# Kernel optimization log

Measured on AMD Instinct MI355X. Metric: run time of the kernel, lower is better.

## Reference

```python
import jax, jax.numpy as jnp
import numpy as np

N = 100000          # number of active sparse points
GRID = 800          # coordinate grid extent (2D)
KS = 9              # 3x3 kernel offsets
C_IN = 24
C_HID = 144         # round(24 * 6)
C_OUT = 24
EPS = 1e-5


def _build_kernel_map():
    """Build MinkowskiEngine-style kernel map for a 3x3 stride-1 channelwise conv.
    Returns (in_idx, out_idx, off_id), each [KS*N] int32. Invalid (no neighbor)
    entries point to sentinel row N so the padded gather/scatter is a no-op."""
    rng = np.random.default_rng(0)
    flat = rng.choice(GRID * GRID, size=N, replace=False)  # unique 2D coords
    ys, xs = flat // GRID, flat % GRID
    coord_to_idx = -np.ones(GRID * GRID, dtype=np.int64)
    coord_to_idx[flat] = np.arange(N)
    in_chunks, out_chunks, off_chunks = [], [], []
    pts = np.arange(N, dtype=np.int64)
    k = 0
    for dy in (-1, 0, 1):
        for dx in (-1, 0, 1):
            ny, nx = ys + dy, xs + dx
            inside = (ny >= 0) & (ny < GRID) & (nx >= 0) & (nx < GRID)
            nflat = np.clip(ny, 0, GRID - 1) * GRID + np.clip(nx, 0, GRID - 1)
            nidx = np.where(inside, coord_to_idx[nflat], -1)
            valid = nidx >= 0
            in_chunks.append(np.where(valid, nidx, N))
            out_chunks.append(np.where(valid, pts, N))
            off_chunks.append(np.full(N, k, dtype=np.int64))
            k += 1
    in_idx = np.concatenate(in_chunks).astype(np.int32)
    out_idx = np.concatenate(out_chunks).astype(np.int32)
    off_id = np.concatenate(off_chunks).astype(np.int32)
    return in_idx, out_idx, off_id


def setup_inputs() -> dict:
    key = jax.random.key(0)
    ks = jax.random.split(key, 4)
    in_idx, out_idx, off_id = _build_kernel_map()
    return {
        "feats": jax.random.normal(ks[0], (N, C_IN), jnp.float32),
        "w1": jax.random.normal(ks[1], (C_IN, C_HID), jnp.float32) * 0.1,
        "g1": jnp.ones((C_HID,), jnp.float32),
        "b1": jnp.zeros((C_HID,), jnp.float32),
        "w2": jax.random.normal(ks[2], (KS, C_HID), jnp.float32) * 0.1,
        "g2": jnp.ones((C_HID,), jnp.float32),
        "b2": jnp.zeros((C_HID,), jnp.float32),
        "w3": jax.random.normal(ks[3], (C_HID, C_OUT), jnp.float32) * 0.1,
        "g3": jnp.ones((C_OUT,), jnp.float32),
        "b3": jnp.zeros((C_OUT,), jnp.float32),
        "in_idx": jnp.asarray(in_idx),
        "out_idx": jnp.asarray(out_idx),
        "off_id": jnp.asarray(off_id),
    }


def _bn(x, g, b):
    # MinkowskiBatchNorm forward (training mode): per-channel stats over points
    m = jnp.mean(x, axis=0)
    v = jnp.var(x, axis=0)
    return (x - m) * jax.lax.rsqrt(v + EPS) * g + b


def _relu6(x):
    return jnp.clip(x, 0.0, 6.0)


def _channelwise_conv3x3(x, w2, in_idx, out_idx, off_id):
    # gather-multiply-scatter: out[p, c] = sum_k w2[k, c] * x[nbr_k(p), c]
    xp = jnp.concatenate([x, jnp.zeros((1, x.shape[1]), x.dtype)], axis=0)  # sentinel row
    contrib = xp[in_idx] * w2[off_id]                     # [KS*N, C_HID]
    out = jnp.zeros((N + 1, x.shape[1]), x.dtype).at[out_idx].add(contrib)
    return out[:N]


def reference(feats, w1, g1, b1, w2, g2, b2, w3, g3, b3, in_idx, out_idx, off_id):
    x = _relu6(_bn(feats @ w1, g1, b1))                   # 1x1 expand
    x = _relu6(_bn(_channelwise_conv3x3(x, w2, in_idx, out_idx, off_id), g2, b2))
    x = _bn(x @ w3, g3, b3)                               # 1x1 project
    return x + feats                                      # residual (in==out, stride==1)
```

## Files before the change

### kernel.cpp

```cpp
#include <hip/hip_runtime.h>

#define N_PTS 100000
#define KSZ 9
#define C_IN 24
#define C_HID 144
#define C_OUT 24
#define G4_HID 36
#define G4_OUT 6
#define EPSV 1e-5f

#define X1N_OFF   0
#define X1N_SIZE  ((N_PTS + 1) * C_HID)
#define X2_OFF    (X1N_OFF + X1N_SIZE)
#define X2_SIZE   (N_PTS * C_HID)
#define ST_OFF    (X2_OFF + X2_SIZE)
#define MU1_O     (ST_OFF + 0)
#define M1_O      (ST_OFF + 32)
#define SC1_O     (ST_OFF + 640)
#define SH1_O     (ST_OFF + 800)
#define SUM2_O    (ST_OFF + 960)
#define SQ2_O     (ST_OFF + 1120)
#define SC2_O     (ST_OFF + 1280)
#define SH2_O     (ST_OFF + 1440)
#define SUM3_O    (ST_OFF + 1600)
#define SQ3_O     (ST_OFF + 1632)
#define SC3_O     (ST_OFF + 1664)
#define SH3_O     (ST_OFF + 1696)
#define ST_SIZE   1728
#define Y3_OFF    0

__device__ inline float4 f4z() { return make_float4(0.f, 0.f, 0.f, 0.f); }
__device__ inline float4 f4_add(float4 a, float4 b) {
    return make_float4(a.x + b.x, a.y + b.y, a.z + b.z, a.w + b.w);
}
__device__ inline float4 f4_fma4(float4 a, float4 b, float4 c) {
    return make_float4(fmaf(a.x, b.x, c.x), fmaf(a.y, b.y, c.y),
                       fmaf(a.z, b.z, c.z), fmaf(a.w, b.w, c.w));
}
__device__ inline float4 f4_fma_s(float s, float4 b, float4 c) {
    return make_float4(fmaf(s, b.x, c.x), fmaf(s, b.y, c.y),
                       fmaf(s, b.z, c.z), fmaf(s, b.w, c.w));
}
__device__ inline float4 f4_clamp6(float4 a) {
    return make_float4(fminf(fmaxf(a.x, 0.f), 6.f), fminf(fmaxf(a.y, 0.f), 6.f),
                       fminf(fmaxf(a.z, 0.f), 6.f), fminf(fmaxf(a.w, 0.f), 6.f));
}
__device__ inline float f4_get(const float4& v, int e) {
    return e == 0 ? v.x : (e == 1 ? v.y : (e == 2 ? v.z : v.w));
}

__global__ void k_init(float* ws) {
    int t = threadIdx.x;
    for (int i = t; i < ST_SIZE; i += 256) ws[ST_OFF + i] = 0.f;
    if (t < C_HID) ws[X1N_OFF + (size_t)N_PTS * C_HID + t] = 0.f;
}

#define MROWS 128
__device__ inline float task_acc(const float* tile, int cnt, int task) {
    if (task < 576) {
        int i = task / 24, j = task % 24;
        float a = 0.f;
        for (int r = 0; r < cnt; r++) a += tile[r * 24 + i] * tile[r * 24 + j];
        return a;
    }
    int k = task - 576;
    float a = 0.f;
    for (int r = 0; r < cnt; r++) a += tile[r * 24 + k];
    return a;
}
__global__ void k_moments(const float* __restrict__ feats, float* __restrict__ ws) {
    __shared__ float tile[MROWS * C_IN];
    int t = threadIdx.x;
    float acc0 = 0.f, acc1 = 0.f, acc2 = 0.f;
    int nChunks = (N_PTS + MROWS - 1) / MROWS;
    for (int ch = blockIdx.x; ch < nChunks; ch += gridDim.x) {
        int r0 = ch * MROWS;
        int cnt = min(MROWS, N_PTS - r0);
        __syncthreads();
        for (int e = t; e < cnt * C_IN; e += 256) tile[e] = feats[(size_t)r0 * C_IN + e];
        __syncthreads();
        acc0 += task_acc(tile, cnt, t);
        acc1 += task_acc(tile, cnt, t + 256);
        if (t < 88) acc2 += task_acc(tile, cnt, t + 512);
    }
    {
        int task = t;
        atomicAdd(&ws[M1_O + task], acc0);
    }
    {
        int task = t + 256;
        atomicAdd(&ws[M1_O + task], acc1);
    }
    if (t < 88) {
        int task = t + 512;
        if (task < 576) atomicAdd(&ws[M1_O + task], acc2);
        else            atomicAdd(&ws[MU1_O + task - 576], acc2);
    }
}

__global__ void k_fin1(const float* __restrict__ w1, const float* __restrict__ g1,
                       const float* __restrict__ b1, float* __restrict__ ws) {
    int c = threadIdx.x;
    if (c >= C_HID) return;
    float wc[C_IN];
    for (int k = 0; k < C_IN; k++) wc[k] = w1[k * C_HID + c];
    const float invN = 1.f / (float)N_PTS;
    float mean = 0.f;
    for (int k = 0; k < C_IN; k++) mean += ws[MU1_O + k] * wc[k];
    mean *= invN;
    float e2 = 0.f;
    for (int i = 0; i < C_IN; i++) {
        float s = 0.f;
        for (int j = 0; j < C_IN; j++) s += ws[M1_O + i * 24 + j] * wc[j];
        e2 += wc[i] * s;
    }
    e2 *= invN;
    float var = e2 - mean * mean;
    float s1 = g1[c] * rsqrtf(var + EPSV);
    ws[SC1_O + c] = s1;
    ws[SH1_O + c] = b1[c] - mean * s1;
}

__global__ void k_gemm1(const float* __restrict__ feats, const float* __restrict__ w1,
                        float* __restrict__ ws) {
    __shared__ float4 w1s[C_IN * G4_HID];
    __shared__ float4 sc[G4_HID], sh[G4_HID];
    int t = threadIdx.x;
    const float4* w1v = (const float4*)w1;
    for (int e = t; e < C_IN * G4_HID; e += 256) w1s[e] = w1v[e];
    if (t < G4_HID) {
        sc[t] = ((const float4*)(ws + SC1_O))[t];
        sh[t] = ((const float4*)(ws + SH1_O))[t];
    }
    __syncthreads();
    float4* x1v = (float4*)(ws + X1N_OFF);
    const int T = N_PTS * G4_HID;
    for (int tau = blockIdx.x * 256 + t; tau < T; tau += gridDim.x * 256) {
        int p = tau / G4_HID;
        int g = tau % G4_HID;
        const float4* fr = (const float4*)(feats + (size_t)p * C_IN);
        float4 acc = f4z();
#pragma unroll
        for (int q = 0; q < 6; q++) {
            float4 fq = fr[q];
            acc = f4_fma_s(fq.x, w1s[(4 * q + 0) * G4_HID + g], acc);
            acc = f4_fma_s(fq.y, w1s[(4 * q + 1) * G4_HID + g], acc);
            acc = f4_fma_s(fq.z, w1s[(4 * q + 2) * G4_HID + g], acc);
            acc = f4_fma_s(fq.w, w1s[(4 * q + 3) * G4_HID + g], acc);
        }
        x1v[tau] = f4_clamp6(f4_fma4(acc, sc[g], sh[g]));
    }
}

__global__ void k_conv(const float* __restrict__ w2, const int* __restrict__ in_idx,
                       float* __restrict__ ws) {
    __shared__ float4 w2s[KSZ * G4_HID];
    __shared__ float lsum[C_HID], lsq[C_HID];
    int t = threadIdx.x;
    for (int e = t; e < KSZ * G4_HID; e += 256) w2s[e] = ((const float4*)w2)[e];
    if (t < C_HID) { lsum[t] = 0.f; lsq[t] = 0.f; }
    __syncthreads();
    const float4* x1v = (const float4*)(ws + X1N_OFF);
    float4* x2v = (float4*)(ws + X2_OFF);
    bool active = t < 252;
    int pt = t / 36, g = t % 36;
    float4 rs = f4z(), rq = f4z();
    int nChunks = (N_PTS + 6) / 7;
    for (int ch = blockIdx.x; ch < nChunks; ch += gridDim.x) {
        int p = ch * 7 + pt;
        if (active && p < N_PTS) {
            int idxs[KSZ];
#pragma unroll
            for (int k = 0; k < KSZ; k++) idxs[k] = in_idx[k * N_PTS + p];
            float4 acc = f4z();
#pragma unroll
            for (int k = 0; k < KSZ; k++) {
                float4 v = x1v[(size_t)idxs[k] * G4_HID + g];
                acc = f4_fma4(w2s[k * G4_HID + g], v, acc);
            }
            x2v[(size_t)p * G4_HID + g] = acc;
            rs = f4_add(rs, acc);
            rq = f4_fma4(acc, acc, rq);
        }
    }
    if (active) {
        atomicAdd(&lsum[4 * g + 0], rs.x); atomicAdd(&lsum[4 * g + 1], rs.y);
        atomicAdd(&lsum[4 * g + 2], rs.z); atomicAdd(&lsum[4 * g + 3], rs.w);
        atomicAdd(&lsq[4 * g + 0], rq.x);  atomicAdd(&lsq[4 * g + 1], rq.y);
        atomicAdd(&lsq[4 * g + 2], rq.z);  atomicAdd(&lsq[4 * g + 3], rq.w);
    }
    __syncthreads();
    if (t < C_HID) {
        atomicAdd(&ws[SUM2_O + t], lsum[t]);
        atomicAdd(&ws[SQ2_O + t], lsq[t]);
    }
}

__global__ void k_fin2(const float* __restrict__ g2, const float* __restrict__ b2,
                       float* __restrict__ ws) {
    int c = threadIdx.x;
    if (c >= C_HID) return;
    const float invN = 1.f / (float)N_PTS;
    float mean = ws[SUM2_O + c] * invN;
    float var = ws[SQ2_O + c] * invN - mean * mean;
    float s = g2[c] * rsqrtf(var + EPSV);
    ws[SC2_O + c] = s;
    ws[SH2_O + c] = b2[c] - mean * s;
}

__global__ void k_gemm2(const float* __restrict__ w3, float* __restrict__ ws) {
    __shared__ float4 w3s[C_HID * G4_OUT];
    __shared__ float4 sc2[G4_HID], sh2[G4_HID];
    int t = threadIdx.x;
    for (int e = t; e < C_HID * G4_OUT; e += 256) w3s[e] = ((const float4*)w3)[e];
    if (t < G4_HID) {
        sc2[t] = ((const float4*)(ws + SC2_O))[t];
        sh2[t] = ((const float4*)(ws + SH2_O))[t];
    }
    __syncthreads();
    const float4* x2v = (const float4*)(ws + X2_OFF);
    float4* y3v = (float4*)(ws + Y3_OFF);
    int gtid = blockIdx.x * 256 + t;
    int r0 = gtid * 2, r1 = r0 + 1;
    bool v0 = r0 < N_PTS, v1 = r1 < N_PTS;
    float4 a0[G4_OUT], a1[G4_OUT];
#pragma unroll
    for (int c4 = 0; c4 < G4_OUT; c4++) { a0[c4] = f4z(); a1[c4] = f4z(); }
    for (int h4 = 0; h4 < G4_HID; h4++) {
        float4 xa = v0 ? x2v[(size_t)r0 * G4_HID + h4] : f4z();
        float4 xb = v1 ? x2v[(size_t)r1 * G4_HID + h4] : f4z();
        float4 s = sc2[h4], b = sh2[h4];
        xa = f4_clamp6(f4_fma4(xa, s, b));
        xb = f4_clamp6(f4_fma4(xb, s, b));
#pragma unroll
        for (int e = 0; e < 4; e++) {
            int h = h4 * 4 + e;
            float fa = f4_get(xa, e), fb = f4_get(xb, e);
#pragma unroll
            for (int c4 = 0; c4 < G4_OUT; c4++) {
                float4 w = w3s[h * G4_OUT + c4];
                a0[c4] = f4_fma_s(fa, w, a0[c4]);
                a1[c4] = f4_fma_s(fb, w, a1[c4]);
            }
        }
    }
    if (v0) {
#pragma unroll
        for (int c4 = 0; c4 < G4_OUT; c4++) y3v[(size_t)r0 * G4_OUT + c4] = a0[c4];
    }
    if (v1) {
#pragma unroll
        for (int c4 = 0; c4 < G4_OUT; c4++) y3v[(size_t)r1 * G4_OUT + c4] = a1[c4];
    }
}

__global__ void k_red3(float* __restrict__ ws) {
    int t = threadIdx.x;
    const float* y3 = ws + Y3_OFF;
    float rs = 0.f, rq = 0.f;
    const int total = N_PTS * C_OUT;
    for (int e = blockIdx.x * 192 + t; e < total; e += gridDim.x * 192) {
        float v = y3[e];
        rs += v; rq += v * v;
    }
    __shared__ float ls[192], lq[192];
    ls[t] = rs; lq[t] = rq;
    __syncthreads();
    if (t < C_OUT) {
        float s = 0.f, q = 0.f;
        for (int u = t; u < 192; u += C_OUT) { s += ls[u]; q += lq[u]; }
        atomicAdd(&ws[SUM3_O + t], s);
        atomicAdd(&ws[SQ3_O + t], q);
    }
}

__global__ void k_fin3(const float* __restrict__ g3, const float* __restrict__ b3,
                       float* __restrict__ ws) {
    int c = threadIdx.x;
    if (c >= C_OUT) return;
    const float invN = 1.f / (float)N_PTS;
    float mean = ws[SUM3_O + c] * invN;
    float var = ws[SQ3_O + c] * invN - mean * mean;
    float s = g3[c] * rsqrtf(var + EPSV);
    ws[SC3_O + c] = s;
    ws[SH3_O + c] = b3[c] - mean * s;
}

__global__ void k_out(const float* __restrict__ feats, const float* __restrict__ ws,
                      float* __restrict__ out) {
    int t4 = blockIdx.x * 256 + threadIdx.x;
    const int T = N_PTS * G4_OUT;
    if (t4 >= T) return;
    int g = t4 % G4_OUT;
    float4 y = ((const float4*)(ws + Y3_OFF))[t4];
    float4 s = ((const float4*)(ws + SC3_O))[g];
    float4 b = ((const float4*)(ws + SH3_O))[g];
    float4 f = ((const float4*)feats)[t4];
    ((float4*)out)[t4] = f4_add(f4_fma4(y, s, b), f);
}

extern "C" void kernel_launch(void* const* d_in, const int* in_sizes, int n_in,
                              void* d_out, int out_size, void* d_ws, size_t ws_size,
                              hipStream_t stream) {
    const float* feats = (const float*)d_in[0];
    const float* w1 = (const float*)d_in[1];
    const float* g1 = (const float*)d_in[2];
    const float* b1 = (const float*)d_in[3];
    const float* w2 = (const float*)d_in[4];
    const float* g2 = (const float*)d_in[5];
    const float* b2 = (const float*)d_in[6];
    const float* w3 = (const float*)d_in[7];
    const float* g3 = (const float*)d_in[8];
    const float* b3 = (const float*)d_in[9];
    const int* in_idx = (const int*)d_in[10];
    float* ws = (float*)d_ws;
    float* out = (float*)d_out;

    hipLaunchKernelGGL(k_init, dim3(1), dim3(256), 0, stream, ws);
    hipLaunchKernelGGL(k_moments, dim3(256), dim3(256), 0, stream, feats, ws);
    hipLaunchKernelGGL(k_fin1, dim3(1), dim3(192), 0, stream, w1, g1, b1, ws);
    hipLaunchKernelGGL(k_gemm1, dim3(2048), dim3(256), 0, stream, feats, w1, ws);
    hipLaunchKernelGGL(k_conv, dim3(2048), dim3(256), 0, stream, w2, in_idx, ws);
    hipLaunchKernelGGL(k_fin2, dim3(1), dim3(192), 0, stream, g2, b2, ws);
    hipLaunchKernelGGL(k_gemm2, dim3((N_PTS + 511) / 512), dim3(256), 0, stream, w3, ws);
    hipLaunchKernelGGL(k_red3, dim3(512), dim3(192), 0, stream, ws);
    hipLaunchKernelGGL(k_fin3, dim3(1), dim3(64), 0, stream, g3, b3, ws);
    hipLaunchKernelGGL(k_out, dim3((N_PTS * G4_OUT + 255) / 256), dim3(256), 0, stream,
                       feats, ws, out);
}
```

Measured before the change: 281.3 us.

## Store intermediates in fp16, fold BN finalize kernels, prefetch conv indices

The expanded and convolved hidden activations are now stored as fp16 instead of fp32, halving the bytes moved by the gather-heavy conv and by gemm2. The three single-block BN finalize kernels are folded into their consumer kernels, and gemm1 keeps BN-scaled weights in registers with one channel per thread. k_moments reads feats straight from global memory with contiguous row ranges per block, and k_conv software-prefetches the next chunk's neighbor indices and uses nontemporal stores. The cost is lower precision on intermediates and per-block recomputation of the BN scale and shift.

```diff
diff --git a/kernel.cpp b/kernel.cpp
--- a/kernel.cpp
+++ b/kernel.cpp
@@ -1,267 +1,259 @@
 #include <hip/hip_runtime.h>
+#include <hip/hip_fp16.h>
 
 #define N_PTS 100000
 #define KSZ 9
 #define C_IN 24
 #define C_HID 144
 #define C_OUT 24
-#define G4_HID 36
-#define G4_OUT 6
 #define EPSV 1e-5f
 
-#define X1N_OFF   0
-#define X1N_SIZE  ((N_PTS + 1) * C_HID)
-#define X2_OFF    (X1N_OFF + X1N_SIZE)
-#define X2_SIZE   (N_PTS * C_HID)
-#define ST_OFF    (X2_OFF + X2_SIZE)
-#define MU1_O     (ST_OFF + 0)
-#define M1_O      (ST_OFF + 32)
-#define SC1_O     (ST_OFF + 640)
-#define SH1_O     (ST_OFF + 800)
-#define SUM2_O    (ST_OFF + 960)
-#define SQ2_O     (ST_OFF + 1120)
-#define SC2_O     (ST_OFF + 1280)
-#define SH2_O     (ST_OFF + 1440)
-#define SUM3_O    (ST_OFF + 1600)
-#define SQ3_O     (ST_OFF + 1632)
-#define SC3_O     (ST_OFF + 1664)
-#define SH3_O     (ST_OFF + 1696)
-#define ST_SIZE   1728
-#define Y3_OFF    0
+#define X1N_B 0ull
+#define X2_B  28800512ull
+#define ST_B  57600512ull
+#define Y3_B  0ull
+
+#define MU1_F  0
+#define M1_F   32
+#define SUM2_F 640
+#define SQ2_F  800
+#define SUM3_F 960
+#define SQ3_F  992
+#define ST_FLOATS 1024
+
+typedef float f4v __attribute__((ext_vector_type(4)));
 
 __device__ inline float4 f4z() { return make_float4(0.f, 0.f, 0.f, 0.f); }
-__device__ inline float4 f4_add(float4 a, float4 b) {
-    return make_float4(a.x + b.x, a.y + b.y, a.z + b.z, a.w + b.w);
-}
-__device__ inline float4 f4_fma4(float4 a, float4 b, float4 c) {
-    return make_float4(fmaf(a.x, b.x, c.x), fmaf(a.y, b.y, c.y),
-                       fmaf(a.z, b.z, c.z), fmaf(a.w, b.w, c.w));
-}
 __device__ inline float4 f4_fma_s(float s, float4 b, float4 c) {
     return make_float4(fmaf(s, b.x, c.x), fmaf(s, b.y, c.y),
                        fmaf(s, b.z, c.z), fmaf(s, b.w, c.w));
 }
-__device__ inline float4 f4_clamp6(float4 a) {
-    return make_float4(fminf(fmaxf(a.x, 0.f), 6.f), fminf(fmaxf(a.y, 0.f), 6.f),
-                       fminf(fmaxf(a.z, 0.f), 6.f), fminf(fmaxf(a.w, 0.f), 6.f));
-}
-__device__ inline float f4_get(const float4& v, int e) {
-    return e == 0 ? v.x : (e == 1 ? v.y : (e == 2 ? v.z : v.w));
-}
-
-__global__ void k_init(float* ws) {
-    int t = threadIdx.x;
-    for (int i = t; i < ST_SIZE; i += 256) ws[ST_OFF + i] = 0.f;
-    if (t < C_HID) ws[X1N_OFF + (size_t)N_PTS * C_HID + t] = 0.f;
-}
-
-#define MROWS 128
-__device__ inline float task_acc(const float* tile, int cnt, int task) {
-    if (task < 576) {
-        int i = task / 24, j = task % 24;
-        float a = 0.f;
-        for (int r = 0; r < cnt; r++) a += tile[r * 24 + i] * tile[r * 24 + j];
-        return a;
-    }
-    int k = task - 576;
+__device__ inline float clamp6(float x) { return fminf(fmaxf(x, 0.f), 6.f); }
+
+__global__ void k_init(char* wsb) {
+    int t = threadIdx.x;
+    float* STF = (float*)(wsb + ST_B);
+    for (int i = t; i < ST_FLOATS; i += 256) STF[i] = 0.f;
+    float* sent = (float*)(wsb + X1N_B + (size_t)N_PTS * (C_HID * 2));
+    if (t < 72) sent[t] = 0.f;
+}
+
+__global__ void k_moments(const float* __restrict__ feats, char* __restrict__ wsb) {
+    int t = threadIdx.x;
+    float* STF = (float*)(wsb + ST_B);
+    int len = (N_PTS + gridDim.x - 1) / gridDim.x;
+    int r0 = blockIdx.x * len;
+    int r1 = min(r0 + len, N_PTS);
+    if (t >= 600) return;
     float a = 0.f;
-    for (int r = 0; r < cnt; r++) a += tile[r * 24 + k];
-    return a;
-}
-__global__ void k_moments(const float* __restrict__ feats, float* __restrict__ ws) {
-    __shared__ float tile[MROWS * C_IN];
-    int t = threadIdx.x;
-    float acc0 = 0.f, acc1 = 0.f, acc2 = 0.f;
-    int nChunks = (N_PTS + MROWS - 1) / MROWS;
-    for (int ch = blockIdx.x; ch < nChunks; ch += gridDim.x) {
-        int r0 = ch * MROWS;
-        int cnt = min(MROWS, N_PTS - r0);
-        __syncthreads();
-        for (int e = t; e < cnt * C_IN; e += 256) tile[e] = feats[(size_t)r0 * C_IN + e];
-        __syncthreads();
-        acc0 += task_acc(tile, cnt, t);
-        acc1 += task_acc(tile, cnt, t + 256);
-        if (t < 88) acc2 += task_acc(tile, cnt, t + 512);
-    }
-    {
-        int task = t;
-        atomicAdd(&ws[M1_O + task], acc0);
-    }
-    {
-        int task = t + 256;
-        atomicAdd(&ws[M1_O + task], acc1);
-    }
-    if (t < 88) {
-        int task = t + 512;
-        if (task < 576) atomicAdd(&ws[M1_O + task], acc2);
-        else            atomicAdd(&ws[MU1_O + task - 576], acc2);
-    }
-}
-
-__global__ void k_fin1(const float* __restrict__ w1, const float* __restrict__ g1,
-                       const float* __restrict__ b1, float* __restrict__ ws) {
-    int c = threadIdx.x;
-    if (c >= C_HID) return;
-    float wc[C_IN];
-    for (int k = 0; k < C_IN; k++) wc[k] = w1[k * C_HID + c];
-    const float invN = 1.f / (float)N_PTS;
-    float mean = 0.f;
-    for (int k = 0; k < C_IN; k++) mean += ws[MU1_O + k] * wc[k];
-    mean *= invN;
-    float e2 = 0.f;
-    for (int i = 0; i < C_IN; i++) {
-        float s = 0.f;
-        for (int j = 0; j < C_IN; j++) s += ws[M1_O + i * 24 + j] * wc[j];
-        e2 += wc[i] * s;
-    }
-    e2 *= invN;
-    float var = e2 - mean * mean;
-    float s1 = g1[c] * rsqrtf(var + EPSV);
-    ws[SC1_O + c] = s1;
-    ws[SH1_O + c] = b1[c] - mean * s1;
-}
-
-__global__ void k_gemm1(const float* __restrict__ feats, const float* __restrict__ w1,
-                        float* __restrict__ ws) {
-    __shared__ float4 w1s[C_IN * G4_HID];
-    __shared__ float4 sc[G4_HID], sh[G4_HID];
-    int t = threadIdx.x;
-    const float4* w1v = (const float4*)w1;
-    for (int e = t; e < C_IN * G4_HID; e += 256) w1s[e] = w1v[e];
-    if (t < G4_HID) {
-        sc[t] = ((const float4*)(ws + SC1_O))[t];
-        sh[t] = ((const float4*)(ws + SH1_O))[t];
-    }
-    __syncthreads();
-    float4* x1v = (float4*)(ws + X1N_OFF);
-    const int T = N_PTS * G4_HID;
-    for (int tau = blockIdx.x * 256 + t; tau < T; tau += gridDim.x * 256) {
-        int p = tau / G4_HID;
-        int g = tau % G4_HID;
+    if (t < 576) {
+        int i = t / 24, j = t % 24;
+#pragma unroll 4
+        for (int r = r0; r < r1; r++)
+            a = fmaf(feats[(size_t)r * 24 + i], feats[(size_t)r * 24 + j], a);
+        atomicAdd(&STF[M1_F + t], a);
+    } else {
+        int k = t - 576;
+#pragma unroll 4
+        for (int r = r0; r < r1; r++) a += feats[(size_t)r * 24 + k];
+        atomicAdd(&STF[MU1_F + k], a);
+    }
+}
+
+__global__ void __launch_bounds__(576, 5)
+k_gemm1(const float* __restrict__ feats, const float* __restrict__ w1,
+        const float* __restrict__ g1, const float* __restrict__ b1,
+        char* __restrict__ wsb) {
+    __shared__ float scs[C_HID], shs[C_HID];
+    float* STF = (float*)(wsb + ST_B);
+    int t = threadIdx.x;
+    if (t < C_HID) {
+        float wc[C_IN];
+#pragma unroll
+        for (int k = 0; k < C_IN; k++) wc[k] = w1[k * C_HID + t];
+        const float invN = 1.f / (float)N_PTS;
+        float mean = 0.f;
+#pragma unroll
+        for (int k = 0; k < C_IN; k++) mean = fmaf(STF[MU1_F + k], wc[k], mean);
+        mean *= invN;
+        float e2 = 0.f;
+        for (int i = 0; i < C_IN; i++) {
+            float s = 0.f;
+#pragma unroll
+            for (int j = 0; j < C_IN; j++) s = fmaf(STF[M1_F + i * 24 + j], wc[j], s);
+            e2 = fmaf(wc[i], s, e2);
+        }
+        e2 *= invN;
+        float var = e2 - mean * mean;
+        float s1 = g1[t] * rsqrtf(var + EPSV);
+        scs[t] = s1;
+        shs[t] = b1[t] - mean * s1;
+    }
+    __syncthreads();
+    int c = t % C_HID, pg = t / C_HID;
+    float sc = scs[c];
+    float sh = shs[c];
+    float wreg[C_IN];
+#pragma unroll
+    for (int k = 0; k < C_IN; k++) wreg[k] = w1[k * C_HID + c] * sc;
+    __half* x1h = (__half*)(wsb + X1N_B);
+    for (int p = blockIdx.x * 4 + pg; p < N_PTS; p += gridDim.x * 4) {
         const float4* fr = (const float4*)(feats + (size_t)p * C_IN);
-        float4 acc = f4z();
+        float acc = sh;
 #pragma unroll
         for (int q = 0; q < 6; q++) {
-            float4 fq = fr[q];
-            acc = f4_fma_s(fq.x, w1s[(4 * q + 0) * G4_HID + g], acc);
-            acc = f4_fma_s(fq.y, w1s[(4 * q + 1) * G4_HID + g], acc);
-            acc = f4_fma_s(fq.z, w1s[(4 * q + 2) * G4_HID + g], acc);
-            acc = f4_fma_s(fq.w, w1s[(4 * q + 3) * G4_HID + g], acc);
-        }
-        x1v[tau] = f4_clamp6(f4_fma4(acc, sc[g], sh[g]));
+            float4 f = fr[q];
+            acc = fmaf(f.x, wreg[4 * q + 0], acc);
+            acc = fmaf(f.y, wreg[4 * q + 1], acc);
+            acc = fmaf(f.z, wreg[4 * q + 2], acc);
+            acc = fmaf(f.w, wreg[4 * q + 3], acc);
+        }
+        x1h[(size_t)p * C_HID + c] = __float2half_rn(clamp6(acc));
     }
 }
 
 __global__ void k_conv(const float* __restrict__ w2, const int* __restrict__ in_idx,
-                       float* __restrict__ ws) {
-    __shared__ float4 w2s[KSZ * G4_HID];
+                       char* __restrict__ wsb) {
+    __shared__ float w2s[KSZ * C_HID];
     __shared__ float lsum[C_HID], lsq[C_HID];
-    int t = threadIdx.x;
-    for (int e = t; e < KSZ * G4_HID; e += 256) w2s[e] = ((const float4*)w2)[e];
+    float* STF = (float*)(wsb + ST_B);
+    int t = threadIdx.x;
+    for (int e = t; e < KSZ * C_HID; e += 256) w2s[e] = w2[e];
     if (t < C_HID) { lsum[t] = 0.f; lsq[t] = 0.f; }
     __syncthreads();
-    const float4* x1v = (const float4*)(ws + X1N_OFF);
-    float4* x2v = (float4*)(ws + X2_OFF);
-    bool active = t < 252;
-    int pt = t / 36, g = t % 36;
-    float4 rs = f4z(), rq = f4z();
-    int nChunks = (N_PTS + 6) / 7;
-    for (int ch = blockIdx.x; ch < nChunks; ch += gridDim.x) {
-        int p = ch * 7 + pt;
-        if (active && p < N_PTS) {
-            int idxs[KSZ];
-#pragma unroll
-            for (int k = 0; k < KSZ; k++) idxs[k] = in_idx[k * N_PTS + p];
-            float4 acc = f4z();
-#pragma unroll
-            for (int k = 0; k < KSZ; k++) {
-                float4 v = x1v[(size_t)idxs[k] * G4_HID + g];
-                acc = f4_fma4(w2s[k * G4_HID + g], v, acc);
+    const __half* x1h = (const __half*)(wsb + X1N_B);
+    __half* x2h = (__half*)(wsb + X2_B);
+    const bool act = t < 252;
+    int pt = t / 18, g = t % 18, c0 = g * 8;
+    float rs[8], rq[8];
+#pragma unroll
+    for (int j = 0; j < 8; j++) { rs[j] = 0.f; rq[j] = 0.f; }
+    const int nChunks = (N_PTS + 13) / 14;
+    int ch = (int)blockIdx.x;
+    int p = ch * 14 + pt;
+    bool ok = act && p < N_PTS;
+    int idxs[KSZ];
+#pragma unroll
+    for (int k = 0; k < KSZ; k++) idxs[k] = ok ? in_idx[k * N_PTS + p] : N_PTS;
+    while (ch < nChunks) {
+        float4 vv[KSZ];
+#pragma unroll
+        for (int k = 0; k < KSZ; k++)
+            vv[k] = *(const float4*)(x1h + (size_t)idxs[k] * C_HID + c0);
+        int chn = ch + (int)gridDim.x;
+        int pn = chn * 14 + pt;
+        bool okn = act && chn < nChunks && pn < N_PTS;
+        int idxn[KSZ];
+#pragma unroll
+        for (int k = 0; k < KSZ; k++) idxn[k] = okn ? in_idx[k * N_PTS + pn] : N_PTS;
+        float acc[8];
+#pragma unroll
+        for (int j = 0; j < 8; j++) acc[j] = 0.f;
+#pragma unroll
+        for (int k = 0; k < KSZ; k++) {
+            union { float4 f; __half2 h[4]; } u;
+            u.f = vv[k];
+#pragma unroll
+            for (int jj = 0; jj < 4; jj++) {
+                float2 x = __half22float2(u.h[jj]);
+                acc[2 * jj]     = fmaf(w2s[k * C_HID + c0 + 2 * jj],     x.x, acc[2 * jj]);
+                acc[2 * jj + 1] = fmaf(w2s[k * C_HID + c0 + 2 * jj + 1], x.y, acc[2 * jj + 1]);
             }
-            x2v[(size_t)p * G4_HID + g] = acc;
-            rs = f4_add(rs, acc);
-            rq = f4_fma4(acc, acc, rq);
-        }
-    }
-    if (active) {
-        atomicAdd(&lsum[4 * g + 0], rs.x); atomicAdd(&lsum[4 * g + 1], rs.y);
-        atomicAdd(&lsum[4 * g + 2], rs.z); atomicAdd(&lsum[4 * g + 3], rs.w);
-        atomicAdd(&lsq[4 * g + 0], rq.x);  atomicAdd(&lsq[4 * g + 1], rq.y);
-        atomicAdd(&lsq[4 * g + 2], rq.z);  atomicAdd(&lsq[4 * g + 3], rq.w);
+        }
+        if (ok) {
+            union { f4v f; __half2 h[4]; } o;
+#pragma unroll
+            for (int jj = 0; jj < 4; jj++)
+                o.h[jj] = __float22half2_rn(make_float2(acc[2 * jj], acc[2 * jj + 1]));
+            __builtin_nontemporal_store(o.f, (f4v*)(x2h + (size_t)p * C_HID + c0));
+#pragma unroll
+            for (int j = 0; j < 8; j++) {
+                rs[j] += acc[j];
+                rq[j] = fmaf(acc[j], acc[j], rq[j]);
+            }
+        }
+        ch = chn; p = pn; ok = okn;
+#pragma unroll
+        for (int k = 0; k < KSZ; k++) idxs[k] = idxn[k];
+    }
+    if (act) {
+#pragma unroll
+        for (int j = 0; j < 8; j++) {
+            atomicAdd(&lsum[c0 + j], rs[j]);
+            atomicAdd(&lsq[c0 + j], rq[j]);
+        }
     }
     __syncthreads();
     if (t < C_HID) {
-        atomicAdd(&ws[SUM2_O + t], lsum[t]);
-        atomicAdd(&ws[SQ2_O + t], lsq[t]);
-    }
-}
-
-__global__ void k_fin2(const float* __restrict__ g2, const float* __restrict__ b2,
-                       float* __restrict__ ws) {
-    int c = threadIdx.x;
-    if (c >= C_HID) return;
-    const float invN = 1.f / (float)N_PTS;
-    float mean = ws[SUM2_O + c] * invN;
-    float var = ws[SQ2_O + c] * invN - mean * mean;
-    float s = g2[c] * rsqrtf(var + EPSV);
-    ws[SC2_O + c] = s;
-    ws[SH2_O + c] = b2[c] - mean * s;
-}
-
-__global__ void k_gemm2(const float* __restrict__ w3, float* __restrict__ ws) {
-    __shared__ float4 w3s[C_HID * G4_OUT];
-    __shared__ float4 sc2[G4_HID], sh2[G4_HID];
-    int t = threadIdx.x;
-    for (int e = t; e < C_HID * G4_OUT; e += 256) w3s[e] = ((const float4*)w3)[e];
-    if (t < G4_HID) {
-        sc2[t] = ((const float4*)(ws + SC2_O))[t];
-        sh2[t] = ((const float4*)(ws + SH2_O))[t];
-    }
-    __syncthreads();
-    const float4* x2v = (const float4*)(ws + X2_OFF);
-    float4* y3v = (float4*)(ws + Y3_OFF);
-    int gtid = blockIdx.x * 256 + t;
-    int r0 = gtid * 2, r1 = r0 + 1;
-    bool v0 = r0 < N_PTS, v1 = r1 < N_PTS;
-    float4 a0[G4_OUT], a1[G4_OUT];
-#pragma unroll
-    for (int c4 = 0; c4 < G4_OUT; c4++) { a0[c4] = f4z(); a1[c4] = f4z(); }
-    for (int h4 = 0; h4 < G4_HID; h4++) {
-        float4 xa = v0 ? x2v[(size_t)r0 * G4_HID + h4] : f4z();
-        float4 xb = v1 ? x2v[(size_t)r1 * G4_HID + h4] : f4z();
-        float4 s = sc2[h4], b = sh2[h4];
-        xa = f4_clamp6(f4_fma4(xa, s, b));
-        xb = f4_clamp6(f4_fma4(xb, s, b));
-#pragma unroll
-        for (int e = 0; e < 4; e++) {
-            int h = h4 * 4 + e;
-            float fa = f4_get(xa, e), fb = f4_get(xb, e);
-#pragma unroll
-            for (int c4 = 0; c4 < G4_OUT; c4++) {
-                float4 w = w3s[h * G4_OUT + c4];
-                a0[c4] = f4_fma_s(fa, w, a0[c4]);
-                a1[c4] = f4_fma_s(fb, w, a1[c4]);
-            }
-        }
-    }
-    if (v0) {
-#pragma unroll
-        for (int c4 = 0; c4 < G4_OUT; c4++) y3v[(size_t)r0 * G4_OUT + c4] = a0[c4];
-    }
-    if (v1) {
-#pragma unroll
-        for (int c4 = 0; c4 < G4_OUT; c4++) y3v[(size_t)r1 * G4_OUT + c4] = a1[c4];
-    }
-}
-
-__global__ void k_red3(float* __restrict__ ws) {
-    int t = threadIdx.x;
-    const float* y3 = ws + Y3_OFF;
+        atomicAdd(&STF[SUM2_F + t], lsum[t]);
+        atomicAdd(&STF[SQ2_F + t], lsq[t]);
+    }
+}
+
+__global__ void k_gemm2(const float* __restrict__ w3, const float* __restrict__ g2,
+                        const float* __restrict__ b2, char* __restrict__ wsb) {
+    __shared__ float4 w3s[C_HID * 6];
+    __shared__ float4 sc2v[C_HID / 4], sh2v[C_HID / 4];
+    float* STF = (float*)(wsb + ST_B);
+    int t = threadIdx.x;
+    for (int e = t; e < C_HID * 6; e += 256) w3s[e] = ((const float4*)w3)[e];
+    if (t < C_HID) {
+        const float invN = 1.f / (float)N_PTS;
+        float mean = STF[SUM2_F + t] * invN;
+        float var = STF[SQ2_F + t] * invN - mean * mean;
+        float s = g2[t] * rsqrtf(var + EPSV);
+        ((float*)sc2v)[t] = s;
+        ((float*)sh2v)[t] = b2[t] - mean * s;
+    }
+    __syncthreads();
+    int r = blockIdx.x * 256 + t;
+    if (r >= N_PTS) return;
+    const float4* x2v = (const float4*)(wsb + X2_B + (size_t)r * (C_HID * 2));
+    float4 a[6];
+#pragma unroll
+    for (int c4 = 0; c4 < 6; c4++) a[c4] = f4z();
+#pragma unroll 6
+    for (int h8 = 0; h8 < 18; h8++) {
+        union { float4 f; __half2 h[4]; } u;
+        u.f = x2v[h8];
+        float4 s0 = sc2v[2 * h8], s1 = sc2v[2 * h8 + 1];
+        float4 b0 = sh2v[2 * h8], b1 = sh2v[2 * h8 + 1];
+        float2 x0 = __half22float2(u.h[0]);
+        float2 x1 = __half22float2(u.h[1]);
+        float2 x2 = __half22float2(u.h[2]);
+        float2 x3 = __half22float2(u.h[3]);
+        float xs[8];
+        xs[0] = clamp6(fmaf(x0.x, s0.x, b0.x));
+        xs[1] = clamp6(fmaf(x0.y, s0.y, b0.y));
+        xs[2] = clamp6(fmaf(x1.x, s0.z, b0.z));
+        xs[3] = clamp6(fmaf(x1.y, s0.w, b0.w));
+        xs[4] = clamp6(fmaf(x2.x, s1.x, b1.x));
+        xs[5] = clamp6(fmaf(x2.y, s1.y, b1.y));
+        xs[6] = clamp6(fmaf(x3.x, s1.z, b1.z));
+        xs[7] = clamp6(fmaf(x3.y, s1.w, b1.w));
+#pragma unroll
+        for (int j = 0; j < 8; j++) {
+            int h = h8 * 8 + j;
+#pragma unroll
+            for (int c4 = 0; c4 < 6; c4++)
+                a[c4] = f4_fma_s(xs[j], w3s[h * 6 + c4], a[c4]);
+        }
+    }
+    float4* y3v = (float4*)(wsb + Y3_B) + (size_t)r * 6;
+#pragma unroll
+    for (int c4 = 0; c4 < 6; c4++) y3v[c4] = a[c4];
+}
+
+__global__ void k_red3(char* __restrict__ wsb) {
+    int t = threadIdx.x;
+    const float* y3 = (const float*)(wsb + Y3_B);
+    float* STF = (float*)(wsb + ST_B);
     float rs = 0.f, rq = 0.f;
     const int total = N_PTS * C_OUT;
     for (int e = blockIdx.x * 192 + t; e < total; e += gridDim.x * 192) {
         float v = y3[e];
-        rs += v; rq += v * v;
+        rs += v;
+        rq = fmaf(v, v, rq);
     }
     __shared__ float ls[192], lq[192];
     ls[t] = rs; lq[t] = rq;
@@ -269,34 +261,37 @@
     if (t < C_OUT) {
         float s = 0.f, q = 0.f;
         for (int u = t; u < 192; u += C_OUT) { s += ls[u]; q += lq[u]; }
-        atomicAdd(&ws[SUM3_O + t], s);
-        atomicAdd(&ws[SQ3_O + t], q);
-    }
-}
-
-__global__ void k_fin3(const float* __restrict__ g3, const float* __restrict__ b3,
-                       float* __restrict__ ws) {
-    int c = threadIdx.x;
-    if (c >= C_OUT) return;
-    const float invN = 1.f / (float)N_PTS;
-    float mean = ws[SUM3_O + c] * invN;
-    float var = ws[SQ3_O + c] * invN - mean * mean;
-    float s = g3[c] * rsqrtf(var + EPSV);
-    ws[SC3_O + c] = s;
-    ws[SH3_O + c] = b3[c] - mean * s;
-}
-
-__global__ void k_out(const float* __restrict__ feats, const float* __restrict__ ws,
+        atomicAdd(&STF[SUM3_F + t], s);
+        atomicAdd(&STF[SQ3_F + t], q);
+    }
+}
+
+__global__ void k_out(const float* __restrict__ feats, const float* __restrict__ g3,
+                      const float* __restrict__ b3, const char* __restrict__ wsb,
                       float* __restrict__ out) {
-    int t4 = blockIdx.x * 256 + threadIdx.x;
-    const int T = N_PTS * G4_OUT;
-    if (t4 >= T) return;
-    int g = t4 % G4_OUT;
-    float4 y = ((const float4*)(ws + Y3_OFF))[t4];
-    float4 s = ((const float4*)(ws + SC3_O))[g];
-    float4 b = ((const float4*)(ws + SH3_O))[g];
-    float4 f = ((const float4*)feats)[t4];
-    ((float4*)out)[t4] = f4_add(f4_fma4(y, s, b), f);
+    __shared__ float s3[C_OUT], h3[C_OUT];
+    const float* STF = (const float*)(wsb + ST_B);
+    int t = threadIdx.x;
+    if (t < C_OUT) {
+        const float invN = 1.f / (float)N_PTS;
+        float mean = STF[SUM3_F + t] * invN;
+        float var = STF[SQ3_F + t] * invN - mean * mean;
+        float s = g3[t] * rsqrtf(var + EPSV);
+        s3[t] = s;
+        h3[t] = b3[t] - mean * s;
+    }
+    __syncthreads();
+    int tau = blockIdx.x * 256 + t;
+    if (tau >= N_PTS * 6) return;
+    int c = (tau % 6) * 4;
+    float4 y = ((const float4*)(wsb + Y3_B))[tau];
+    float4 f = ((const float4*)feats)[tau];
+    float4 o;
+    o.x = fmaf(y.x, s3[c + 0], h3[c + 0]) + f.x;
+    o.y = fmaf(y.y, s3[c + 1], h3[c + 1]) + f.y;
+    o.z = fmaf(y.z, s3[c + 2], h3[c + 2]) + f.z;
+    o.w = fmaf(y.w, s3[c + 3], h3[c + 3]) + f.w;
+    ((float4*)out)[tau] = o;
 }
 
 extern "C" void kernel_launch(void* const* d_in, const int* in_sizes, int n_in,
@@ -313,18 +308,15 @@
     const float* g3 = (const float*)d_in[8];
     const float* b3 = (const float*)d_in[9];
     const int* in_idx = (const int*)d_in[10];
-    float* ws = (float*)d_ws;
+    char* wsb = (char*)d_ws;
     float* out = (float*)d_out;
 
-    hipLaunchKernelGGL(k_init, dim3(1), dim3(256), 0, stream, ws);
-    hipLaunchKernelGGL(k_moments, dim3(256), dim3(256), 0, stream, feats, ws);
-    hipLaunchKernelGGL(k_fin1, dim3(1), dim3(192), 0, stream, w1, g1, b1, ws);
-    hipLaunchKernelGGL(k_gemm1, dim3(2048), dim3(256), 0, stream, feats, w1, ws);
-    hipLaunchKernelGGL(k_conv, dim3(2048), dim3(256), 0, stream, w2, in_idx, ws);
-    hipLaunchKernelGGL(k_fin2, dim3(1), dim3(192), 0, stream, g2, b2, ws);
-    hipLaunchKernelGGL(k_gemm2, dim3((N_PTS + 511) / 512), dim3(256), 0, stream, w3, ws);
-    hipLaunchKernelGGL(k_red3, dim3(512), dim3(192), 0, stream, ws);
-    hipLaunchKernelGGL(k_fin3, dim3(1), dim3(64), 0, stream, g3, b3, ws);
-    hipLaunchKernelGGL(k_out, dim3((N_PTS * G4_OUT + 255) / 256), dim3(256), 0, stream,
-                       feats, ws, out);
-}
+    hipLaunchKernelGGL(k_init, dim3(1), dim3(256), 0, stream, wsb);
+    hipLaunchKernelGGL(k_moments, dim3(256), dim3(640), 0, stream, feats, wsb);
+    hipLaunchKernelGGL(k_gemm1, dim3(1024), dim3(576), 0, stream, feats, w1, g1, b1, wsb);
+    hipLaunchKernelGGL(k_conv, dim3(2048), dim3(256), 0, stream, w2, in_idx, wsb);
+    hipLaunchKernelGGL(k_gemm2, dim3((N_PTS + 255) / 256), dim3(256), 0, stream, w3, g2, b2, wsb);
+    hipLaunchKernelGGL(k_red3, dim3(512), dim3(192), 0, stream, wsb);
+    hipLaunchKernelGGL(k_out, dim3((N_PTS * 6 + 255) / 256), dim3(256), 0, stream,
+                       feats, g3, b3, wsb, out);
+}
```

New measurement: 292.6 us. 1.04x slower.
